# Optimization experiments

Measured on AMD Instinct MI355X. Metric: run time of the kernel, lower is better.

## Reference

```python
import jax, jax.numpy as jnp
import numpy as np

B = 8192
DV = 768   # visual_input_size
DT = 768   # text_input_size
E = 8      # num_experts
D = 1024   # expert_output_size
G = 2 * D  # gate_input_size
EPS = 1e-5


def setup_inputs() -> dict:
    key = jax.random.key(0)
    ks = jax.random.split(key, 14)
    s = lambda fan_in: 1.0 / np.sqrt(fan_in)
    return {
        "visual_features": jax.random.normal(ks[0], (B, DV), dtype=jnp.float32),
        "text_features": jax.random.normal(ks[1], (B, DT), dtype=jnp.float32),
        "vis_w": jax.random.uniform(ks[2], (DV, D), jnp.float32, -s(DV), s(DV)),
        "vis_b": jax.random.uniform(ks[3], (D,), jnp.float32, -s(DV), s(DV)),
        "txt_w": jax.random.uniform(ks[4], (DT, D), jnp.float32, -s(DT), s(DT)),
        "txt_b": jax.random.uniform(ks[5], (D,), jnp.float32, -s(DT), s(DT)),
        "gate_w": jax.random.uniform(ks[6], (G, E), jnp.float32, -s(G), s(G)),
        "gate_b": jax.random.uniform(ks[7], (E,), jnp.float32, -s(G), s(G)),
        "w1": jax.random.uniform(ks[8], (E, G, D), jnp.float32, -s(G), s(G)),
        "b1": jax.random.uniform(ks[9], (E, D), jnp.float32, -s(G), s(G)),
        "w2": jax.random.uniform(ks[10], (E, D, D), jnp.float32, -s(D), s(D)),
        "b2": jax.random.uniform(ks[11], (E, D), jnp.float32, -s(D), s(D)),
        "ln_g": jnp.ones((E, D), dtype=jnp.float32),
        "ln_b": jnp.zeros((E, D), dtype=jnp.float32),
    }


def reference(visual_features, text_features, vis_w, vis_b, txt_w, txt_b,
              gate_w, gate_b, w1, b1, w2, b2, ln_g, ln_b):
    # Projections + concat -> combined features [B, 2D]
    pv = visual_features @ vis_w + vis_b
    pt = text_features @ txt_w + txt_b
    combined = jnp.concatenate([pv, pt], axis=1)

    # Gate (dropout is identity at inference)
    gate_probs = jax.nn.softmax(combined @ gate_w + gate_b, axis=1)  # [B, E]

    # All experts as batched GEMMs: [B,G] x [E,G,D] -> [B,E,D]
    h = jnp.einsum('bg,egd->bed', combined, w1) + b1
    h = jax.nn.gelu(h, approximate=False)  # torch nn.GELU default = exact erf
    h = jnp.einsum('bed,edo->beo', h, w2) + b2

    # Per-expert LayerNorm over last dim
    mu = jnp.mean(h, axis=-1, keepdims=True)
    var = jnp.mean(jnp.square(h - mu), axis=-1, keepdims=True)
    h = (h - mu) * jax.lax.rsqrt(var + EPS) * ln_g + ln_b

    # Gated reduction over experts
    return jnp.einsum('bed,be->bd', h, gate_probs)
```

## Files before the change

### kernel.cpp

```cpp
#include <hip/hip_runtime.h>
#include <hip/hip_bf16.h>
#include <math.h>

#define BM 128
#define BN 128
#define BK 64

typedef __bf16 bf16x8_t __attribute__((ext_vector_type(8)));
typedef __bf16 bf16x4_t __attribute__((ext_vector_type(4)));
typedef float f32x16_t __attribute__((ext_vector_type(16)));

static __device__ __forceinline__ float bf2f(__bf16 b) {
    unsigned short s = __builtin_bit_cast(unsigned short, b);
    unsigned int u = ((unsigned int)s) << 16;
    return __builtin_bit_cast(float, u);
}
static __device__ __forceinline__ __bf16 f2bf(float f) {
    unsigned int u = __builtin_bit_cast(unsigned int, f);
    unsigned int r = (u + 0x7fffu + ((u >> 16) & 1u)) >> 16;
    return __builtin_bit_cast(__bf16, (unsigned short)r);
}
static __device__ __forceinline__ float gelu_fast(float x) {
    const float s = x * (0.7978845608f + 0.0356774081f * x * x);
    const float e = __expf(-2.0f * s);
    return x * __builtin_amdgcn_rcpf(1.0f + e);
}

#define GLDS16(gp, lp)                                                                   \
    __builtin_amdgcn_global_load_lds((const __attribute__((address_space(1))) void*)(gp), \
                                     (__attribute__((address_space(3))) void*)(lp), 16, 0, 0)

__global__ __launch_bounds__(256) void frag_cast(const float* __restrict__ in,
                                                 __bf16* __restrict__ out,
                                                 int K, int N,
                                                 size_t inStride, size_t outStride,
                                                 const float* __restrict__ vb,
                                                 const float* __restrict__ tb,
                                                 const float* __restrict__ b1,
                                                 float* __restrict__ b1t) {
    in += (size_t)blockIdx.z * inStride;
    out += (size_t)blockIdx.z * outStride;
    __shared__ float tile[64][65];
    __shared__ float pb[4][64];
    const int k0 = blockIdx.x * 64, n0 = blockIdx.y * 64;
    const int tid = threadIdx.x;
    const int r = tid >> 4, c4 = (tid & 15) * 4;
#pragma unroll
    for (int p = 0; p < 4; ++p) {
        const float4 v = *(const float4*)&in[(size_t)(k0 + r + p * 16) * N + n0 + c4];
        tile[r + p * 16][c4 + 0] = v.x;
        tile[r + p * 16][c4 + 1] = v.y;
        tile[r + p * 16][c4 + 2] = v.z;
        tile[r + p * 16][c4 + 3] = v.w;
    }
    __syncthreads();
    if (b1t) {
        const int n = tid & 63, kq = tid >> 6;
        float p = 0.f;
#pragma unroll
        for (int rr = 0; rr < 16; ++rr) {
            const int kg = k0 + kq * 16 + rr;
            const float bv = (kg < 1024) ? vb[kg] : tb[kg - 1024];
            p += bv * tile[kq * 16 + rr][n];
        }
        pb[kq][n] = p;
    }
    const int c = tid >> 5, nn0 = (tid & 31) * 2;
#pragma unroll
    for (int t = 0; t < 2; ++t) {
        const int nn = nn0 + t;
        bf16x8_t v;
#pragma unroll
        for (int j = 0; j < 8; ++j) v[j] = f2bf(tile[c * 8 + j][nn]);
        *(bf16x8_t*)&out[((size_t)(k0 >> 3) + c) * N * 8 + (size_t)(n0 + nn) * 8] = v;
    }
    if (b1t) {
        __syncthreads();
        if (tid < 64) {
            float s = pb[0][tid] + pb[1][tid] + pb[2][tid] + pb[3][tid];
            if (k0 == 0) s += b1[(size_t)blockIdx.z * 1024 + n0 + tid];
            atomicAdd(&b1t[(size_t)blockIdx.z * 1024 + n0 + tid], s);
        }
    }
}

__global__ __launch_bounds__(256) void cast2_kernel(const float* __restrict__ a,
                                                    const float* __restrict__ b,
                                                    __bf16* __restrict__ out) {
    __shared__ __align__(16) __bf16 lds[8 * 1032];
    const int ct = blockIdx.x, mb = blockIdx.y, m = blockIdx.z, tid = threadIdx.x;
    const int c0 = ct * 64;
    const float* src = (m ? b : a) + (size_t)mb * 128 * 1024 + c0;
#pragma unroll
    for (int k = 0; k < 8; ++k) {
        const int f = tid + k * 256;
        const int row = f >> 4, c4 = f & 15;
        const float4 v = *(const float4*)(src + (size_t)row * 1024 + c4 * 4);
        __bf16* d = lds + (c4 >> 1) * 1032 + row * 8 + (c4 & 1) * 4;
        d[0] = f2bf(v.x); d[1] = f2bf(v.y); d[2] = f2bf(v.z); d[3] = f2bf(v.w);
    }
    __syncthreads();
    __bf16* dst = out + (size_t)m * 786432 + (size_t)mb * 131072 + (size_t)(c0 >> 3) * 1024;
#pragma unroll
    for (int k = 0; k < 4; ++k) {
        const int g = tid + k * 256;
        const int ch = g >> 7, row = g & 127;
        const bf16x8_t v = *(const bf16x8_t*)(lds + ch * 1032 + row * 8);
        *(bf16x8_t*)(dst + (size_t)ch * 1024 + row * 8) = v;
    }
}

__global__ __launch_bounds__(256) void cast_acat(const float* __restrict__ vis,
                                                 const float* __restrict__ txt,
                                                 __bf16* __restrict__ out) {
    __shared__ __align__(16) __bf16 lds[8 * 1032];
    const int ct = blockIdx.x, mb = blockIdx.y, tid = threadIdx.x;
    const int c0 = ct * 64;
    const float* src = (c0 < 768) ? vis + (size_t)mb * 128 * 768 + c0
                                  : txt + (size_t)mb * 128 * 768 + (c0 - 768);
#pragma unroll
    for (int k = 0; k < 8; ++k) {
        const int f = tid + k * 256;
        const int row = f >> 4, c4 = f & 15;
        const float4 v = *(const float4*)(src + (size_t)row * 768 + c4 * 4);
        __bf16* d = lds + (c4 >> 1) * 1032 + row * 8 + (c4 & 1) * 4;
        d[0] = f2bf(v.x); d[1] = f2bf(v.y); d[2] = f2bf(v.z); d[3] = f2bf(v.w);
    }
    __syncthreads();
    __bf16* dst = out + (size_t)mb * 196608 + (size_t)(c0 >> 3) * 1024;
#pragma unroll
    for (int k = 0; k < 4; ++k) {
        const int g = tid + k * 256;
        const int ch = g >> 7, row = g & 127;
        const bf16x8_t v = *(const bf16x8_t*)(lds + ch * 1032 + row * 8);
        *(bf16x8_t*)(dst + (size_t)ch * 1024 + row * 8) = v;
    }
}

#define MFMA32(a, b, c) __builtin_amdgcn_mfma_f32_32x32x16_bf16(a, b, c, 0, 0, 0)

template <int ACT, int PACK>
static __device__ __forceinline__ void gemm_core(const __bf16* __restrict__ A, int K,
                                                 const __bf16* __restrict__ Bt, int Bn,
                                                 const float* __restrict__ bias,
                                                 __bf16* __restrict__ C, int ldc,
                                                 int bm, int bn, __bf16* As) {
    const int tid = threadIdx.x;
    const int lane = tid & 63, wave = tid >> 6;
    const int wm = wave >> 1, wn = wave & 1;
    const int l = lane & 31, hi = lane >> 5;

    const __bf16* ag = A + (size_t)bm * K * 128 + (size_t)tid * 8;
    __bf16* asl = As + tid * 8;

    const __bf16* base_a = As + hi * 1024 + (wm * 64 + l) * 8;

    const size_t Bn8 = (size_t)Bn * 8;
    const __bf16* bbase = Bt + (size_t)hi * Bn8 + (size_t)(bn * BN + wn * 64 + l) * 8;
    const size_t bAdv = 8 * Bn8;

    f32x16_t acc[2][2] = {};

    const int nk = K / BK;
    for (int kt = 0; kt < nk; ++kt) {
        bf16x8_t bfr[4][2];
#pragma unroll
        for (int s = 0; s < 4; ++s) {
            bfr[s][0] = *(const bf16x8_t*)(bbase + (size_t)(2 * s) * Bn8);
            bfr[s][1] = *(const bf16x8_t*)(bbase + (size_t)(2 * s) * Bn8 + 256);
        }
        GLDS16(ag, asl);
        GLDS16(ag + 2048, asl + 2048);
        GLDS16(ag + 4096, asl + 4096);
        GLDS16(ag + 6144, asl + 6144);
        ag += 8192;
        bbase += bAdv;
        __syncthreads();
#pragma unroll
        for (int s = 0; s < 4; ++s) {
            const bf16x8_t a0 = *(const bf16x8_t*)(base_a + s * 2048);
            const bf16x8_t a1 = *(const bf16x8_t*)(base_a + s * 2048 + 256);
            acc[0][0] = MFMA32(a0, bfr[s][0], acc[0][0]);
            acc[0][1] = MFMA32(a0, bfr[s][1], acc[0][1]);
            acc[1][0] = MFMA32(a1, bfr[s][0], acc[1][0]);
            acc[1][1] = MFMA32(a1, bfr[s][1], acc[1][1]);
        }
        __syncthreads();
    }

    const int colbase = bn * BN + wn * 64 + l;
    const int rowbase = bm * BM + wm * 64 + 4 * hi;
#pragma unroll
    for (int ni = 0; ni < 2; ++ni) {
        const int col = colbase + ni * 32;
        const float bv = (PACK == 1) ? 0.0f : bias[col];
#pragma unroll
        for (int mi = 0; mi < 2; ++mi) {
#pragma unroll
            for (int v = 0; v < 16; ++v) {
                const int row = rowbase + mi * 32 + (v & 3) + 8 * (v >> 2);
                float x = acc[mi][ni][v] + bv;
                if (ACT == 1) x = gelu_fast(x);
                if (PACK == 1) {
                    C[((size_t)(row >> 3)) * (size_t)ldc * 8 + (size_t)col * 8 + (row & 7)] = f2bf(x);
                } else if (PACK == 2) {
                    C[(size_t)(row >> 7) * (size_t)ldc * 128 + (size_t)(col >> 3) * 1024 +
                      (size_t)(row & 127) * 8 + (col & 7)] = f2bf(x);
                } else {
                    C[(size_t)row * ldc + col] = f2bf(x);
                }
            }
        }
    }
}

template <int ACT, int PACK>
__global__ __launch_bounds__(256, 4) void gemm_bt(const __bf16* __restrict__ Ab, int K, size_t strideAe,
                                                  const __bf16* __restrict__ Bb, int Bn, size_t strideBe,
                                                  const float* __restrict__ biasb, size_t strideBiasE,
                                                  __bf16* __restrict__ Cb, int ldc, size_t strideCe) {
    __shared__ __bf16 As[BM * BK];
    gemm_core<ACT, PACK>(Ab + (size_t)blockIdx.z * strideAe, K,
                         Bb + (size_t)blockIdx.z * strideBe, Bn,
                         biasb + (size_t)blockIdx.z * strideBiasE,
                         Cb + (size_t)blockIdx.z * strideCe, ldc,
                         blockIdx.x, blockIdx.y, As);
}

__global__ __launch_bounds__(256, 4) void gemm_premul(const __bf16* __restrict__ wbf,
                                                      const __bf16* __restrict__ w1t,
                                                      __bf16* __restrict__ w1cat) {
    __shared__ __bf16 As[BM * BK];
    const int e = blockIdx.z & 7, hf = blockIdx.z >> 3;
    gemm_core<0, 1>(wbf + (size_t)hf * 786432, 1024,
                    w1t + (size_t)e * 2048 * 1024 + (size_t)hf * 128 * 1024 * 8, 1024,
                    nullptr,
                    w1cat + (size_t)e * 1536 * 1024 + (size_t)hf * 96 * 1024 * 8, 1024,
                    blockIdx.x, blockIdx.y, As);
}

__global__ __launch_bounds__(256) void gcat_kernel(const float* __restrict__ vis_w,
                                                   const float* __restrict__ txt_w,
                                                   const float* __restrict__ vis_b,
                                                   const float* __restrict__ txt_b,
                                                   const float* __restrict__ gw,
                                                   const float* __restrict__ gb,
                                                   float* __restrict__ gcat) {
    const int v = blockIdx.x, tid = threadIdx.x;
    const int lane = tid & 63, wv = tid >> 6;
    float a[8] = {0, 0, 0, 0, 0, 0, 0, 0};
    if (v < 1536) {
        const float* wr = (v < 768) ? vis_w + (size_t)v * 1024 : txt_w + (size_t)(v - 768) * 1024;
        const int dbase = (v < 768) ? 0 : 1024;
        for (int d = tid; d < 1024; d += 256) {
            const float c = wr[d];
            const float4* g4 = (const float4*)(gw + (size_t)(dbase + d) * 8);
            const float4 x = g4[0], y = g4[1];
            a[0] += c * x.x; a[1] += c * x.y; a[2] += c * x.z; a[3] += c * x.w;
            a[4] += c * y.x; a[5] += c * y.y; a[6] += c * y.z; a[7] += c * y.w;
        }
    } else {
        for (int d = tid; d < 2048; d += 256) {
            const float c = (d < 1024) ? vis_b[d] : txt_b[d - 1024];
            const float4* g4 = (const float4*)(gw + (size_t)d * 8);
            const float4 x = g4[0], y = g4[1];
            a[0] += c * x.x; a[1] += c * x.y; a[2] += c * x.z; a[3] += c * x.w;
            a[4] += c * y.x; a[5] += c * y.y; a[6] += c * y.z; a[7] += c * y.w;
        }
    }
#pragma unroll
    for (int j = 0; j < 8; ++j)
        for (int off = 32; off; off >>= 1) a[j] += __shfl_down(a[j], off, 64);
    __shared__ float red[4][8];
    if (lane == 0) {
#pragma unroll
        for (int j = 0; j < 8; ++j) red[wv][j] = a[j];
    }
    __syncthreads();
    if (tid < 8) {
        float s = red[0][tid] + red[1][tid] + red[2][tid] + red[3][tid];
        if (v == 1536) s += gb[tid];
        gcat[(size_t)v * 8 + tid] = s;
    }
}

__global__ __launch_bounds__(256) void gate_kernel(const __bf16* __restrict__ acat,
                                                   const float* __restrict__ gcat,
                                                   float* __restrict__ gate) {
    const int bid = blockIdx.x, tid = threadIdx.x;
    const int lane = tid & 63, wv = tid >> 6;
    const int mblk = bid >> 1;
    const int rowIn = (bid & 1) * 64 + lane;
    const __bf16* base = acat + (size_t)mblk * 196608 + (size_t)rowIn * 8;
    float a[8] = {0, 0, 0, 0, 0, 0, 0, 0};
    for (int k = 0; k < 48; ++k) {
        const int c = wv + 4 * k;
        const bf16x8_t av = *(const bf16x8_t*)(base + (size_t)c * 1024);
        const float* g = gcat + (size_t)c * 64;
#pragma unroll
        for (int jj = 0; jj < 8; ++jj) {
            const float cf = bf2f(av[jj]);
            const float4 x = *(const float4*)(g + jj * 8);
            const float4 y = *(const float4*)(g + jj * 8 + 4);
            a[0] += cf * x.x; a[1] += cf * x.y; a[2] += cf * x.z; a[3] += cf * x.w;
            a[4] += cf * y.x; a[5] += cf * y.y; a[6] += cf * y.z; a[7] += cf * y.w;
        }
    }
    __shared__ float red[4][64][9];
#pragma unroll
    for (int j = 0; j < 8; ++j) red[wv][lane][j] = a[j];
    __syncthreads();
    if (tid < 64) {
        const float* bg = gcat + 1536 * 8;
        float l[8];
        float m = -1e30f;
#pragma unroll
        for (int j = 0; j < 8; ++j) {
            l[j] = red[0][tid][j] + red[1][tid][j] + red[2][tid][j] + red[3][tid][j] + bg[j];
            m = fmaxf(m, l[j]);
        }
        float s = 0.f;
#pragma unroll
        for (int j = 0; j < 8; ++j) { l[j] = expf(l[j] - m); s += l[j]; }
        const float inv = 1.0f / s;
        const size_t r = (size_t)bid * 64 + tid;
#pragma unroll
        for (int j = 0; j < 8; ++j) gate[r * 8 + j] = l[j] * inv;
    }
}

__global__ __launch_bounds__(256) void ln_out_kernel(const __bf16* __restrict__ h2,
                                                     const float* __restrict__ gate,
                                                     const float* __restrict__ lng,
                                                     const float* __restrict__ lnb,
                                                     float* __restrict__ out,
                                                     int Eg, int g0, int accum) {
    const int lane = threadIdx.x & 63;
    const int b = blockIdx.x * 4 + (threadIdx.x >> 6);
    const int d0 = lane * 4;
    float* orow = out + (size_t)b * 1024 + d0;
    float o[16];
    if (accum) {
#pragma unroll
        for (int q = 0; q < 4; ++q) {
            const float4 p = *(const float4*)(orow + q * 256);
            o[q * 4 + 0] = p.x; o[q * 4 + 1] = p.y; o[q * 4 + 2] = p.z; o[q * 4 + 3] = p.w;
        }
    } else {
#pragma unroll
        for (int j = 0; j < 16; ++j) o[j] = 0.f;
    }
    for (int e = 0; e < Eg; ++e) {
        const __bf16* hp = h2 + ((size_t)e * 8192 + b) * 1024 + d0;
        float v[16];
#pragma unroll
        for (int q = 0; q < 4; ++q) {
            const bf16x4_t hv = *(const bf16x4_t*)(hp + q * 256);
            v[q * 4 + 0] = bf2f(hv[0]); v[q * 4 + 1] = bf2f(hv[1]);
            v[q * 4 + 2] = bf2f(hv[2]); v[q * 4 + 3] = bf2f(hv[3]);
        }
        float s = 0.f, ss = 0.f;
#pragma unroll
        for (int j = 0; j < 16; ++j) { s += v[j]; ss += v[j] * v[j]; }
#pragma unroll
        for (int off = 32; off; off >>= 1) {
            s += __shfl_xor(s, off, 64);
            ss += __shfl_xor(ss, off, 64);
        }
        const float mu = s * (1.0f / 1024.0f);
        const float var = ss * (1.0f / 1024.0f) - mu * mu;
        const float rstd = rsqrtf(var + 1e-5f);
        const float w = gate[(size_t)b * 8 + g0 + e];
        const float* gg = lng + (size_t)(g0 + e) * 1024 + d0;
        const float* bb = lnb + (size_t)(g0 + e) * 1024 + d0;
#pragma unroll
        for (int q = 0; q < 4; ++q) {
            const float4 g4 = *(const float4*)(gg + q * 256);
            const float4 b4 = *(const float4*)(bb + q * 256);
            o[q * 4 + 0] += w * ((v[q * 4 + 0] - mu) * rstd * g4.x + b4.x);
            o[q * 4 + 1] += w * ((v[q * 4 + 1] - mu) * rstd * g4.y + b4.y);
            o[q * 4 + 2] += w * ((v[q * 4 + 2] - mu) * rstd * g4.z + b4.z);
            o[q * 4 + 3] += w * ((v[q * 4 + 3] - mu) * rstd * g4.w + b4.w);
        }
    }
#pragma unroll
    for (int q = 0; q < 4; ++q)
        *(float4*)(orow + q * 256) = make_float4(o[q * 4], o[q * 4 + 1], o[q * 4 + 2], o[q * 4 + 3]);
}

extern "C" void kernel_launch(void* const* d_in, const int* in_sizes, int n_in,
                              void* d_out, int out_size, void* d_ws, size_t ws_size,
                              hipStream_t stream) {
    (void)in_sizes; (void)n_in; (void)out_size;
    const float* visual = (const float*)d_in[0];
    const float* text   = (const float*)d_in[1];
    const float* vis_w  = (const float*)d_in[2];
    const float* vis_b  = (const float*)d_in[3];
    const float* txt_w  = (const float*)d_in[4];
    const float* txt_b  = (const float*)d_in[5];
    const float* gate_w = (const float*)d_in[6];
    const float* gate_b = (const float*)d_in[7];
    const float* w1     = (const float*)d_in[8];
    const float* b1     = (const float*)d_in[9];
    const float* w2     = (const float*)d_in[10];
    const float* b2     = (const float*)d_in[11];
    const float* ln_g   = (const float*)d_in[12];
    const float* ln_b   = (const float*)d_in[13];
    float* out = (float*)d_out;

    const size_t B = 8192, DV = 768, D = 1024, G = 2048, E = 8, KC = 1536;

    char* ws = (char*)d_ws;
    size_t o = 0;
    auto alloc = [&](size_t bytes) { size_t r = o; o = (o + bytes + 255) & ~(size_t)255; return r; };
    const size_t off_wbf   = alloc(2 * DV * D * 2);
    const size_t off_w1cat = alloc(E * KC * D * 2);
    const size_t off_w2t   = alloc(E * D * D * 2);
    const size_t off_b1t   = alloc(E * D * 4);
    const size_t off_gcat  = alloc((KC * E + E) * 4);
    const size_t off_gate  = alloc(B * E * 4);
    const size_t off_acat  = alloc(B * KC * 2);
    const size_t fixedEnd = o;
    const size_t w1tBytes = E * G * D * 2;

    int Eg = 1;
    {
        const int cand[4] = {8, 4, 2, 1};
        for (int c = 0; c < 4; ++c) {
            size_t h2b = 2 * (size_t)cand[c] * B * D * 2;
            size_t dyn = h2b > w1tBytes ? h2b : w1tBytes;
            if (fixedEnd + dyn <= ws_size || cand[c] == 1) { Eg = cand[c]; break; }
        }
    }

    __bf16* wbf   = (__bf16*)(ws + off_wbf);
    __bf16* w1cat = (__bf16*)(ws + off_w1cat);
    __bf16* w2t   = (__bf16*)(ws + off_w2t);
    float*  b1t   = (float*)(ws + off_b1t);
    float*  gcat  = (float*)(ws + off_gcat);
    float*  gate  = (float*)(ws + off_gate);
    __bf16* acat  = (__bf16*)(ws + off_acat);
    __bf16* w1t   = (__bf16*)(ws + fixedEnd);
    __bf16* h1    = (__bf16*)(ws + fixedEnd);
    __bf16* h2    = h1 + (size_t)Eg * B * D;

    cast2_kernel<<<dim3(16, 6, 2), 256, 0, stream>>>(vis_w, txt_w, wbf);
    cast_acat<<<dim3(24, 64), 256, 0, stream>>>(visual, text, acat);

    hipMemsetAsync(b1t, 0, E * D * 4, stream);
    frag_cast<<<dim3(G / 64, D / 64, E), 256, 0, stream>>>(w1, w1t, (int)G, (int)D, G * D, G * D,
                                                           vis_b, txt_b, b1, b1t);
    frag_cast<<<dim3(D / 64, D / 64, E), 256, 0, stream>>>(w2, w2t, (int)D, (int)D, D * D, D * D,
                                                           nullptr, nullptr, nullptr, nullptr);

    gemm_premul<<<dim3(768 / BM, D / BN, 16), 256, 0, stream>>>(wbf, w1t, w1cat);

    gcat_kernel<<<1537, 256, 0, stream>>>(vis_w, txt_w, vis_b, txt_b, gate_w, gate_b, gcat);

    gate_kernel<<<128, 256, 0, stream>>>(acat, gcat, gate);

    const int ng = 8 / Eg;
    for (int g = 0; g < ng; ++g) {
        const int g0 = g * Eg;
        gemm_bt<1, 2><<<dim3(B / BM, D / BN, Eg), 256, 0, stream>>>(
            acat, (int)KC, 0, w1cat + (size_t)g0 * KC * D, (int)D, KC * D,
            b1t + (size_t)g0 * D, D, h1, (int)D, B * D);
        gemm_bt<0, 0><<<dim3(B / BM, D / BN, Eg), 256, 0, stream>>>(
            h1, (int)D, B * D, w2t + (size_t)g0 * D * D, (int)D, D * D,
            b2 + (size_t)g0 * D, D, h2, (int)D, B * D);
        ln_out_kernel<<<(int)(B / 4), 256, 0, stream>>>(h2, gate, ln_g, ln_b, out, Eg, g0, g > 0 ? 1 : 0);
    }
}
```

Before: 717.4 us.

## Fuse front-end cast kernels into one launch and swizzle GEMM block order

Folds the weight casts, activation cast, w1/w2 fragment transposes and gate-weight folding into a single front_kernel that dispatches on block index. It also merges the premultiply GEMM with the gate softmax kernel. The expert GEMMs now launch on a 1D grid with a block-index swizzle so neighbouring blocks share B tiles. The aim is to cut launch overhead and idle gaps between small kernels and to improve L2 reuse in the big GEMMs, at the cost of larger LDS per block in the fused kernel and divergent block roles.

```diff
diff --git a/kernel.cpp b/kernel.cpp
--- a/kernel.cpp
+++ b/kernel.cpp
@@ -30,40 +30,34 @@
     __builtin_amdgcn_global_load_lds((const __attribute__((address_space(1))) void*)(gp), \
                                      (__attribute__((address_space(3))) void*)(lp), 16, 0, 0)
 
-__global__ __launch_bounds__(256) void frag_cast(const float* __restrict__ in,
+
+template <bool DOBIAS>
+static __device__ __forceinline__ void frag_body(const float* __restrict__ in,
                                                  __bf16* __restrict__ out,
-                                                 int K, int N,
-                                                 size_t inStride, size_t outStride,
+                                                 int N, int k0, int n0, int tid,
+                                                 float* tile , float* pb ,
                                                  const float* __restrict__ vb,
                                                  const float* __restrict__ tb,
-                                                 const float* __restrict__ b1,
-                                                 float* __restrict__ b1t) {
-    in += (size_t)blockIdx.z * inStride;
-    out += (size_t)blockIdx.z * outStride;
-    __shared__ float tile[64][65];
-    __shared__ float pb[4][64];
-    const int k0 = blockIdx.x * 64, n0 = blockIdx.y * 64;
-    const int tid = threadIdx.x;
+                                                 const float* __restrict__ b1e,
+                                                 float* __restrict__ b1te) {
     const int r = tid >> 4, c4 = (tid & 15) * 4;
 #pragma unroll
     for (int p = 0; p < 4; ++p) {
         const float4 v = *(const float4*)&in[(size_t)(k0 + r + p * 16) * N + n0 + c4];
-        tile[r + p * 16][c4 + 0] = v.x;
-        tile[r + p * 16][c4 + 1] = v.y;
-        tile[r + p * 16][c4 + 2] = v.z;
-        tile[r + p * 16][c4 + 3] = v.w;
+        float* t = tile + (r + p * 16) * 65 + c4;
+        t[0] = v.x; t[1] = v.y; t[2] = v.z; t[3] = v.w;
     }
     __syncthreads();
-    if (b1t) {
+    if (DOBIAS) {
         const int n = tid & 63, kq = tid >> 6;
         float p = 0.f;
 #pragma unroll
         for (int rr = 0; rr < 16; ++rr) {
             const int kg = k0 + kq * 16 + rr;
             const float bv = (kg < 1024) ? vb[kg] : tb[kg - 1024];
-            p += bv * tile[kq * 16 + rr][n];
-        }
-        pb[kq][n] = p;
+            p += bv * tile[(kq * 16 + rr) * 65 + n];
+        }
+        pb[kq * 64 + n] = p;
     }
     const int c = tid >> 5, nn0 = (tid & 31) * 2;
 #pragma unroll
@@ -71,36 +65,31 @@
         const int nn = nn0 + t;
         bf16x8_t v;
 #pragma unroll
-        for (int j = 0; j < 8; ++j) v[j] = f2bf(tile[c * 8 + j][nn]);
+        for (int j = 0; j < 8; ++j) v[j] = f2bf(tile[(c * 8 + j) * 65 + nn]);
         *(bf16x8_t*)&out[((size_t)(k0 >> 3) + c) * N * 8 + (size_t)(n0 + nn) * 8] = v;
     }
-    if (b1t) {
+    if (DOBIAS) {
         __syncthreads();
         if (tid < 64) {
-            float s = pb[0][tid] + pb[1][tid] + pb[2][tid] + pb[3][tid];
-            if (k0 == 0) s += b1[(size_t)blockIdx.z * 1024 + n0 + tid];
-            atomicAdd(&b1t[(size_t)blockIdx.z * 1024 + n0 + tid], s);
-        }
-    }
-}
-
-__global__ __launch_bounds__(256) void cast2_kernel(const float* __restrict__ a,
-                                                    const float* __restrict__ b,
-                                                    __bf16* __restrict__ out) {
-    __shared__ __align__(16) __bf16 lds[8 * 1032];
-    const int ct = blockIdx.x, mb = blockIdx.y, m = blockIdx.z, tid = threadIdx.x;
-    const int c0 = ct * 64;
-    const float* src = (m ? b : a) + (size_t)mb * 128 * 1024 + c0;
+            float s = pb[tid] + pb[64 + tid] + pb[128 + tid] + pb[192 + tid];
+            if (k0 == 0) s += b1e[n0 + tid];
+            atomicAdd(&b1te[n0 + tid], s);
+        }
+    }
+}
+
+static __device__ __forceinline__ void castpack_body(const float* __restrict__ src,
+                                                     int srcLd, __bf16* __restrict__ dst,
+                                                     int tid, __bf16* lds ) {
 #pragma unroll
     for (int k = 0; k < 8; ++k) {
         const int f = tid + k * 256;
         const int row = f >> 4, c4 = f & 15;
-        const float4 v = *(const float4*)(src + (size_t)row * 1024 + c4 * 4);
+        const float4 v = *(const float4*)(src + (size_t)row * srcLd + c4 * 4);
         __bf16* d = lds + (c4 >> 1) * 1032 + row * 8 + (c4 & 1) * 4;
         d[0] = f2bf(v.x); d[1] = f2bf(v.y); d[2] = f2bf(v.z); d[3] = f2bf(v.w);
     }
     __syncthreads();
-    __bf16* dst = out + (size_t)m * 786432 + (size_t)mb * 131072 + (size_t)(c0 >> 3) * 1024;
 #pragma unroll
     for (int k = 0; k < 4; ++k) {
         const int g = tid + k * 256;
@@ -110,30 +99,85 @@
     }
 }
 
-__global__ __launch_bounds__(256) void cast_acat(const float* __restrict__ vis,
-                                                 const float* __restrict__ txt,
-                                                 __bf16* __restrict__ out) {
-    __shared__ __align__(16) __bf16 lds[8 * 1032];
-    const int ct = blockIdx.x, mb = blockIdx.y, tid = threadIdx.x;
-    const int c0 = ct * 64;
-    const float* src = (c0 < 768) ? vis + (size_t)mb * 128 * 768 + c0
-                                  : txt + (size_t)mb * 128 * 768 + (c0 - 768);
-#pragma unroll
-    for (int k = 0; k < 8; ++k) {
-        const int f = tid + k * 256;
-        const int row = f >> 4, c4 = f & 15;
-        const float4 v = *(const float4*)(src + (size_t)row * 768 + c4 * 4);
-        __bf16* d = lds + (c4 >> 1) * 1032 + row * 8 + (c4 & 1) * 4;
-        d[0] = f2bf(v.x); d[1] = f2bf(v.y); d[2] = f2bf(v.z); d[3] = f2bf(v.w);
-    }
-    __syncthreads();
-    __bf16* dst = out + (size_t)mb * 196608 + (size_t)(c0 >> 3) * 1024;
-#pragma unroll
-    for (int k = 0; k < 4; ++k) {
-        const int g = tid + k * 256;
-        const int ch = g >> 7, row = g & 127;
-        const bf16x8_t v = *(const bf16x8_t*)(lds + ch * 1032 + row * 8);
-        *(bf16x8_t*)(dst + (size_t)ch * 1024 + row * 8) = v;
+__global__ __launch_bounds__(256) void front_kernel(
+    const float* __restrict__ visual, const float* __restrict__ text,
+    const float* __restrict__ vis_w, const float* __restrict__ txt_w,
+    const float* __restrict__ w1, const float* __restrict__ w2,
+    const float* __restrict__ vis_b, const float* __restrict__ txt_b,
+    const float* __restrict__ b1,
+    const float* __restrict__ gw, const float* __restrict__ gb,
+    __bf16* __restrict__ wbf, __bf16* __restrict__ acat,
+    __bf16* __restrict__ w1t, __bf16* __restrict__ w2t,
+    float* __restrict__ b1t, float* __restrict__ gcat) {
+    __shared__ __align__(16) float smem[64 * 65 + 256];
+    const int id = blockIdx.x;
+    const int tid = threadIdx.x;
+    if (id < 192) {
+        __bf16* lds = (__bf16*)smem;
+        const int m = id / 96, r2 = id % 96;
+        const int mb = r2 >> 4, ct = r2 & 15;
+        const int c0 = ct * 64;
+        const float* src = (m ? txt_w : vis_w) + (size_t)mb * 128 * 1024 + c0;
+        __bf16* dst = wbf + (size_t)m * 786432 + (size_t)mb * 131072 + (size_t)(c0 >> 3) * 1024;
+        castpack_body(src, 1024, dst, tid, lds);
+    } else if (id < 1728) {
+        __bf16* lds = (__bf16*)smem;
+        const int i = id - 192;
+        const int ct = i % 24, mb = i / 24;
+        const int c0 = ct * 64;
+        const float* src = (c0 < 768) ? visual + (size_t)mb * 128 * 768 + c0
+                                      : text + (size_t)mb * 128 * 768 + (c0 - 768);
+        __bf16* dst = acat + (size_t)mb * 196608 + (size_t)(c0 >> 3) * 1024;
+        castpack_body(src, 768, dst, tid, lds);
+    } else if (id < 5824) {
+        const int i = id - 1728;
+        const int kx = i & 31, ny = (i >> 5) & 15, e = i >> 9;
+        frag_body<true>(w1 + (size_t)e * 2048 * 1024, w1t + (size_t)e * 2048 * 1024,
+                        1024, kx * 64, ny * 64, tid, smem, smem + 64 * 65,
+                        vis_b, txt_b, b1 + (size_t)e * 1024, b1t + (size_t)e * 1024);
+    } else if (id < 7872) {
+        const int i = id - 5824;
+        const int kx = i & 15, ny = (i >> 4) & 15, e = i >> 8;
+        frag_body<false>(w2 + (size_t)e * 1024 * 1024, w2t + (size_t)e * 1024 * 1024,
+                         1024, kx * 64, ny * 64, tid, smem, smem + 64 * 65,
+                         nullptr, nullptr, nullptr, nullptr);
+    } else {
+        const int v = id - 7872;
+        const int lane = tid & 63, wv = tid >> 6;
+        float a[8] = {0, 0, 0, 0, 0, 0, 0, 0};
+        if (v < 1536) {
+            const float* wr = (v < 768) ? vis_w + (size_t)v * 1024 : txt_w + (size_t)(v - 768) * 1024;
+            const int dbase = (v < 768) ? 0 : 1024;
+            for (int d = tid; d < 1024; d += 256) {
+                const float c = wr[d];
+                const float4* g4 = (const float4*)(gw + (size_t)(dbase + d) * 8);
+                const float4 x = g4[0], y = g4[1];
+                a[0] += c * x.x; a[1] += c * x.y; a[2] += c * x.z; a[3] += c * x.w;
+                a[4] += c * y.x; a[5] += c * y.y; a[6] += c * y.z; a[7] += c * y.w;
+            }
+        } else {
+            for (int d = tid; d < 2048; d += 256) {
+                const float c = (d < 1024) ? vis_b[d] : txt_b[d - 1024];
+                const float4* g4 = (const float4*)(gw + (size_t)d * 8);
+                const float4 x = g4[0], y = g4[1];
+                a[0] += c * x.x; a[1] += c * x.y; a[2] += c * x.z; a[3] += c * x.w;
+                a[4] += c * y.x; a[5] += c * y.y; a[6] += c * y.z; a[7] += c * y.w;
+            }
+        }
+#pragma unroll
+        for (int j = 0; j < 8; ++j)
+            for (int off = 32; off; off >>= 1) a[j] += __shfl_down(a[j], off, 64);
+        float* red = smem;
+        if (lane == 0) {
+#pragma unroll
+            for (int j = 0; j < 8; ++j) red[wv * 8 + j] = a[j];
+        }
+        __syncthreads();
+        if (tid < 8) {
+            float s = red[tid] + red[8 + tid] + red[16 + tid] + red[24 + tid];
+            if (v == 1536) s += gb[tid];
+            gcat[(size_t)v * 8 + tid] = s;
+        }
     }
 }
 
@@ -220,112 +264,79 @@
                                                   const float* __restrict__ biasb, size_t strideBiasE,
                                                   __bf16* __restrict__ Cb, int ldc, size_t strideCe) {
     __shared__ __bf16 As[BM * BK];
-    gemm_core<ACT, PACK>(Ab + (size_t)blockIdx.z * strideAe, K,
-                         Bb + (size_t)blockIdx.z * strideBe, Bn,
-                         biasb + (size_t)blockIdx.z * strideBiasE,
-                         Cb + (size_t)blockIdx.z * strideCe, ldc,
-                         blockIdx.x, blockIdx.y, As);
-}
-
-__global__ __launch_bounds__(256, 4) void gemm_premul(const __bf16* __restrict__ wbf,
+    const int bid = blockIdx.x;
+    const int cpx = gridDim.x >> 3;
+    const int swz = (bid & 7) * cpx + (bid >> 3);
+    const int bm = swz & 63, bn = (swz >> 6) & 7, z = swz >> 9;
+    gemm_core<ACT, PACK>(Ab + (size_t)z * strideAe, K,
+                         Bb + (size_t)z * strideBe, Bn,
+                         biasb + (size_t)z * strideBiasE,
+                         Cb + (size_t)z * strideCe, ldc, bm, bn, As);
+}
+
+__global__ __launch_bounds__(256, 4) void premul_gate(const __bf16* __restrict__ wbf,
                                                       const __bf16* __restrict__ w1t,
-                                                      __bf16* __restrict__ w1cat) {
-    __shared__ __bf16 As[BM * BK];
-    const int e = blockIdx.z & 7, hf = blockIdx.z >> 3;
-    gemm_core<0, 1>(wbf + (size_t)hf * 786432, 1024,
-                    w1t + (size_t)e * 2048 * 1024 + (size_t)hf * 128 * 1024 * 8, 1024,
-                    nullptr,
-                    w1cat + (size_t)e * 1536 * 1024 + (size_t)hf * 96 * 1024 * 8, 1024,
-                    blockIdx.x, blockIdx.y, As);
-}
-
-__global__ __launch_bounds__(256) void gcat_kernel(const float* __restrict__ vis_w,
-                                                   const float* __restrict__ txt_w,
-                                                   const float* __restrict__ vis_b,
-                                                   const float* __restrict__ txt_b,
-                                                   const float* __restrict__ gw,
-                                                   const float* __restrict__ gb,
-                                                   float* __restrict__ gcat) {
-    const int v = blockIdx.x, tid = threadIdx.x;
-    const int lane = tid & 63, wv = tid >> 6;
-    float a[8] = {0, 0, 0, 0, 0, 0, 0, 0};
-    if (v < 1536) {
-        const float* wr = (v < 768) ? vis_w + (size_t)v * 1024 : txt_w + (size_t)(v - 768) * 1024;
-        const int dbase = (v < 768) ? 0 : 1024;
-        for (int d = tid; d < 1024; d += 256) {
-            const float c = wr[d];
-            const float4* g4 = (const float4*)(gw + (size_t)(dbase + d) * 8);
-            const float4 x = g4[0], y = g4[1];
-            a[0] += c * x.x; a[1] += c * x.y; a[2] += c * x.z; a[3] += c * x.w;
-            a[4] += c * y.x; a[5] += c * y.y; a[6] += c * y.z; a[7] += c * y.w;
-        }
+                                                      __bf16* __restrict__ w1cat,
+                                                      const __bf16* __restrict__ acat,
+                                                      const float* __restrict__ gcat,
+                                                      float* __restrict__ gate) {
+    __shared__ __align__(16) __bf16 As[BM * BK];
+    const int id = blockIdx.x;
+    const int tid = threadIdx.x;
+    if (id < 768) {
+        const int swz = (id & 7) * 96 + (id >> 3);
+        const int bm = swz % 6;
+        const int t1 = swz / 6;
+        const int bn = t1 & 7;
+        const int z = t1 >> 3;
+        const int e = z & 7, hf = z >> 3;
+        gemm_core<0, 1>(wbf + (size_t)hf * 786432, 1024,
+                        w1t + (size_t)e * 2048 * 1024 + (size_t)hf * 128 * 1024 * 8, 1024,
+                        nullptr,
+                        w1cat + (size_t)e * 1536 * 1024 + (size_t)hf * 96 * 1024 * 8, 1024,
+                        bm, bn, As);
     } else {
-        for (int d = tid; d < 2048; d += 256) {
-            const float c = (d < 1024) ? vis_b[d] : txt_b[d - 1024];
-            const float4* g4 = (const float4*)(gw + (size_t)d * 8);
-            const float4 x = g4[0], y = g4[1];
-            a[0] += c * x.x; a[1] += c * x.y; a[2] += c * x.z; a[3] += c * x.w;
-            a[4] += c * y.x; a[5] += c * y.y; a[6] += c * y.z; a[7] += c * y.w;
-        }
-    }
-#pragma unroll
-    for (int j = 0; j < 8; ++j)
-        for (int off = 32; off; off >>= 1) a[j] += __shfl_down(a[j], off, 64);
-    __shared__ float red[4][8];
-    if (lane == 0) {
-#pragma unroll
-        for (int j = 0; j < 8; ++j) red[wv][j] = a[j];
-    }
-    __syncthreads();
-    if (tid < 8) {
-        float s = red[0][tid] + red[1][tid] + red[2][tid] + red[3][tid];
-        if (v == 1536) s += gb[tid];
-        gcat[(size_t)v * 8 + tid] = s;
-    }
-}
-
-__global__ __launch_bounds__(256) void gate_kernel(const __bf16* __restrict__ acat,
-                                                   const float* __restrict__ gcat,
-                                                   float* __restrict__ gate) {
-    const int bid = blockIdx.x, tid = threadIdx.x;
-    const int lane = tid & 63, wv = tid >> 6;
-    const int mblk = bid >> 1;
-    const int rowIn = (bid & 1) * 64 + lane;
-    const __bf16* base = acat + (size_t)mblk * 196608 + (size_t)rowIn * 8;
-    float a[8] = {0, 0, 0, 0, 0, 0, 0, 0};
-    for (int k = 0; k < 48; ++k) {
-        const int c = wv + 4 * k;
-        const bf16x8_t av = *(const bf16x8_t*)(base + (size_t)c * 1024);
-        const float* g = gcat + (size_t)c * 64;
-#pragma unroll
-        for (int jj = 0; jj < 8; ++jj) {
-            const float cf = bf2f(av[jj]);
-            const float4 x = *(const float4*)(g + jj * 8);
-            const float4 y = *(const float4*)(g + jj * 8 + 4);
-            a[0] += cf * x.x; a[1] += cf * x.y; a[2] += cf * x.z; a[3] += cf * x.w;
-            a[4] += cf * y.x; a[5] += cf * y.y; a[6] += cf * y.z; a[7] += cf * y.w;
-        }
-    }
-    __shared__ float red[4][64][9];
-#pragma unroll
-    for (int j = 0; j < 8; ++j) red[wv][lane][j] = a[j];
-    __syncthreads();
-    if (tid < 64) {
-        const float* bg = gcat + 1536 * 8;
-        float l[8];
-        float m = -1e30f;
-#pragma unroll
-        for (int j = 0; j < 8; ++j) {
-            l[j] = red[0][tid][j] + red[1][tid][j] + red[2][tid][j] + red[3][tid][j] + bg[j];
-            m = fmaxf(m, l[j]);
-        }
-        float s = 0.f;
-#pragma unroll
-        for (int j = 0; j < 8; ++j) { l[j] = expf(l[j] - m); s += l[j]; }
-        const float inv = 1.0f / s;
-        const size_t r = (size_t)bid * 64 + tid;
-#pragma unroll
-        for (int j = 0; j < 8; ++j) gate[r * 8 + j] = l[j] * inv;
+        const int bid = id - 768;
+        const int lane = tid & 63, wv = tid >> 6;
+        const int mblk = bid >> 1;
+        const int rowIn = (bid & 1) * 64 + lane;
+        const __bf16* base = acat + (size_t)mblk * 196608 + (size_t)rowIn * 8;
+        float a[8] = {0, 0, 0, 0, 0, 0, 0, 0};
+        for (int k = 0; k < 48; ++k) {
+            const int c = wv + 4 * k;
+            const bf16x8_t av = *(const bf16x8_t*)(base + (size_t)c * 1024);
+            const float* g = gcat + (size_t)c * 64;
+#pragma unroll
+            for (int jj = 0; jj < 8; ++jj) {
+                const float cf = bf2f(av[jj]);
+                const float4 x = *(const float4*)(g + jj * 8);
+                const float4 y = *(const float4*)(g + jj * 8 + 4);
+                a[0] += cf * x.x; a[1] += cf * x.y; a[2] += cf * x.z; a[3] += cf * x.w;
+                a[4] += cf * y.x; a[5] += cf * y.y; a[6] += cf * y.z; a[7] += cf * y.w;
+            }
+        }
+        float* red = (float*)As;
+#pragma unroll
+        for (int j = 0; j < 8; ++j) red[(wv * 64 + lane) * 9 + j] = a[j];
+        __syncthreads();
+        if (tid < 64) {
+            const float* bg = gcat + 1536 * 8;
+            float l[8];
+            float m = -1e30f;
+#pragma unroll
+            for (int j = 0; j < 8; ++j) {
+                l[j] = red[tid * 9 + j] + red[(64 + tid) * 9 + j] +
+                       red[(128 + tid) * 9 + j] + red[(192 + tid) * 9 + j] + bg[j];
+                m = fmaxf(m, l[j]);
+            }
+            float s = 0.f;
+#pragma unroll
+            for (int j = 0; j < 8; ++j) { l[j] = expf(l[j] - m); s += l[j]; }
+            const float inv = 1.0f / s;
+            const size_t r = (size_t)bid * 64 + tid;
+#pragma unroll
+            for (int j = 0; j < 8; ++j) gate[r * 8 + j] = l[j] * inv;
+        }
     }
 }
 
@@ -444,28 +455,20 @@
     __bf16* h1    = (__bf16*)(ws + fixedEnd);
     __bf16* h2    = h1 + (size_t)Eg * B * D;
 
-    cast2_kernel<<<dim3(16, 6, 2), 256, 0, stream>>>(vis_w, txt_w, wbf);
-    cast_acat<<<dim3(24, 64), 256, 0, stream>>>(visual, text, acat);
-
     hipMemsetAsync(b1t, 0, E * D * 4, stream);
-    frag_cast<<<dim3(G / 64, D / 64, E), 256, 0, stream>>>(w1, w1t, (int)G, (int)D, G * D, G * D,
-                                                           vis_b, txt_b, b1, b1t);
-    frag_cast<<<dim3(D / 64, D / 64, E), 256, 0, stream>>>(w2, w2t, (int)D, (int)D, D * D, D * D,
-                                                           nullptr, nullptr, nullptr, nullptr);
-
-    gemm_premul<<<dim3(768 / BM, D / BN, 16), 256, 0, stream>>>(wbf, w1t, w1cat);
-
-    gcat_kernel<<<1537, 256, 0, stream>>>(vis_w, txt_w, vis_b, txt_b, gate_w, gate_b, gcat);
-
-    gate_kernel<<<128, 256, 0, stream>>>(acat, gcat, gate);
+    front_kernel<<<9409, 256, 0, stream>>>(visual, text, vis_w, txt_w, w1, w2,
+                                           vis_b, txt_b, b1, gate_w, gate_b,
+                                           wbf, acat, w1t, w2t, b1t, gcat);
+
+    premul_gate<<<896, 256, 0, stream>>>(wbf, w1t, w1cat, acat, gcat, gate);
 
     const int ng = 8 / Eg;
     for (int g = 0; g < ng; ++g) {
         const int g0 = g * Eg;
-        gemm_bt<1, 2><<<dim3(B / BM, D / BN, Eg), 256, 0, stream>>>(
+        gemm_bt<1, 2><<<512 * Eg, 256, 0, stream>>>(
             acat, (int)KC, 0, w1cat + (size_t)g0 * KC * D, (int)D, KC * D,
             b1t + (size_t)g0 * D, D, h1, (int)D, B * D);
-        gemm_bt<0, 0><<<dim3(B / BM, D / BN, Eg), 256, 0, stream>>>(
+        gemm_bt<0, 0><<<512 * Eg, 256, 0, stream>>>(
             h1, (int)D, B * D, w2t + (size_t)g0 * D * D, (int)D, D * D,
             b2 + (size_t)g0 * D, D, h2, (int)D, B * D);
         ln_out_kernel<<<(int)(B / 4), 256, 0, stream>>>(h2, gate, ln_g, ln_b, out, Eg, g0, g > 0 ? 1 : 0);
```

After: 721.7 us. Within noise of the previous version (+0.6%).
